# Kernel tuning notes

Measured on AMD Instinct MI355X. Metric: run time of the kernel, lower is better.

Reference implementation:

```python
import jax, jax.numpy as jnp
import numpy as np

OUT, IN, BLK, RANK = 4096, 4096, 32, 16
N_BLOCKS = IN // BLK  # 128
Q_ZERO = 128.0  # center of unsigned code range, maps codes to signed values


def setup_inputs() -> dict:
    key = jax.random.key(0)
    ks = jax.random.split(key, 6)
    x = jax.random.normal(ks[0], (4, 2048, IN), dtype=jnp.float32)
    # GGML-style block-quantized weight: int codes in blocks of 32 + per-block fp scale
    q_weight = jax.random.randint(ks[1], (OUT, N_BLOCKS, BLK), 0, 256, dtype=jnp.int32)
    scales = jax.random.uniform(ks[2], (OUT, N_BLOCKS), dtype=jnp.float32) * 0.02
    # LoRA patch applied to dequantized weight
    lora_up = jax.random.normal(ks[3], (OUT, RANK), dtype=jnp.float32) * 0.02
    lora_down = jax.random.normal(ks[4], (RANK, IN), dtype=jnp.float32) * 0.02
    bias = jax.random.normal(ks[5], (OUT,), dtype=jnp.float32)
    return {"x": x, "q_weight": q_weight, "scales": scales,
            "lora_up": lora_up, "lora_down": lora_down, "bias": bias}


def reference(x, q_weight, scales, lora_up, lora_down, bias):
    # 1) dequantize: per-block scale * centered int codes -> full fp weight [OUT, IN]
    w = (q_weight.astype(jnp.float32) - Q_ZERO) * scales[:, :, None]
    w = w.reshape(OUT, IN)
    # 2) apply LoRA patch to the dequantized weight (patch function in get_weight)
    w = w + lora_up @ lora_down
    # 3) delegate to the linear forward operation: y = x @ W^T + b
    return jnp.einsum('bsd,od->bso', x, w) + bias
```

## Files before the change

kernel.cpp:

```cpp
#include <hip/hip_runtime.h>
#include <cstdint>
#include <cstddef>

#define M_TOT 8192
#define N_TOT 4096
#define K_TOT 4096
#define RANK  16
#define BM 128
#define BN 128
#define BK 32

typedef float f32x4 __attribute__((ext_vector_type(4)));
typedef __bf16 bf16x8 __attribute__((ext_vector_type(8)));
typedef unsigned short u16x4 __attribute__((ext_vector_type(4)));

__device__ __forceinline__ unsigned short f32_to_bf16(float f) {
    union { float f; uint32_t u; } v; v.f = f;
    uint32_t r = v.u + (0x7fffu + ((v.u >> 16) & 1u));
    return (unsigned short)(r >> 16);
}

__device__ __forceinline__ void gload_lds16(const void* g, void* l) {
    __builtin_amdgcn_global_load_lds(
        (const __attribute__((address_space(1))) void*)g,
        (__attribute__((address_space(3))) void*)l,
        16, 0, 0);
}

__global__ __launch_bounds__(256) void convert_x_kernel(const float* __restrict__ x,
                                                        unsigned short* __restrict__ xb,
                                                        int n4) {
    int i = blockIdx.x * 256 + threadIdx.x;
    if (i >= n4) return;
    float4 v = ((const float4*)x)[i];
    u16x4 o;
    o.x = f32_to_bf16(v.x);
    o.y = f32_to_bf16(v.y);
    o.z = f32_to_bf16(v.z);
    o.w = f32_to_bf16(v.w);
    *(u16x4*)&xb[(size_t)i * 4] = o;
}

__global__ __launch_bounds__(256) void build_w_kernel(const int* __restrict__ q,
                                                      const float* __restrict__ scales,
                                                      const float* __restrict__ up,
                                                      const float* __restrict__ down,
                                                      unsigned short* __restrict__ W) {
    const int o = blockIdx.x;
    const int t = threadIdx.x;
    __shared__ float u[RANK];
    if (t < RANK) u[t] = up[o * RANK + t];
    __syncthreads();

    const int* qrow = q + (size_t)o * K_TOT;
    const float* srow = scales + (size_t)o * (K_TOT / 32);
    float acc[16];
#pragma unroll
    for (int i = 0; i < 16; i++) {
        int kk = t + 256 * i;
        acc[i] = ((float)qrow[kk] - 128.0f) * srow[kk >> 5];
    }
#pragma unroll
    for (int r = 0; r < RANK; r++) {
        float ur = u[r];
        const float* drow = down + (size_t)r * K_TOT;
#pragma unroll
        for (int i = 0; i < 16; i++) acc[i] += ur * drow[t + 256 * i];
    }
    unsigned short* wrow = W + (size_t)o * K_TOT;
#pragma unroll
    for (int i = 0; i < 16; i++) wrow[t + 256 * i] = f32_to_bf16(acc[i]);
}

__global__ __launch_bounds__(256) void gemm_bt_kernel(const unsigned short* __restrict__ A,
                                                      const unsigned short* __restrict__ B,
                                                      const float* __restrict__ bias,
                                                      float* __restrict__ C) {
    __shared__ unsigned short As[BM * BK];
    __shared__ unsigned short Bs[BN * BK];

    const int tid  = threadIdx.x;
    const int wave = tid >> 6;
    const int lane = tid & 63;
    const int wm = wave >> 1;
    const int wn = wave & 1;

    const int tile_m = (int)blockIdx.y * BM;
    const int tile_n = (int)blockIdx.x * BN;

    const int lrow = lane >> 2;
    const int lcol = (lane & 3) * 8;

    const int quad = lane >> 4;
    const int l16  = lane & 15;

    f32x4 acc[4][4];
#pragma unroll
    for (int i = 0; i < 4; i++)
#pragma unroll
        for (int j = 0; j < 4; j++) {
            f32x4 z = {0.f, 0.f, 0.f, 0.f};
            acc[i][j] = z;
        }

    for (int k0 = 0; k0 < K_TOT; k0 += BK) {
#pragma unroll
        for (int j = 0; j < 2; j++) {
            const int r0 = (j * 4 + wave) * 16;
            gload_lds16(A + (size_t)(tile_m + r0 + lrow) * K_TOT + (k0 + lcol), &As[r0 * BK]);
            gload_lds16(B + (size_t)(tile_n + r0 + lrow) * K_TOT + (k0 + lcol), &Bs[r0 * BK]);
        }
        __syncthreads();

        bf16x8 af[4], bfr[4];
#pragma unroll
        for (int mi = 0; mi < 4; mi++)
            af[mi] = *(const bf16x8*)&As[(wm * 64 + mi * 16 + l16) * BK + quad * 8];
#pragma unroll
        for (int ni = 0; ni < 4; ni++)
            bfr[ni] = *(const bf16x8*)&Bs[(wn * 64 + ni * 16 + l16) * BK + quad * 8];

#pragma unroll
        for (int mi = 0; mi < 4; mi++)
#pragma unroll
            for (int ni = 0; ni < 4; ni++)
                acc[mi][ni] = __builtin_amdgcn_mfma_f32_16x16x32_bf16(af[mi], bfr[ni], acc[mi][ni], 0, 0, 0);
        __syncthreads();
    }

#pragma unroll
    for (int ni = 0; ni < 4; ni++) {
        const int col = tile_n + wn * 64 + ni * 16 + l16;
        const float bv = bias[col];
#pragma unroll
        for (int mi = 0; mi < 4; mi++) {
#pragma unroll
            for (int r = 0; r < 4; r++) {
                const int row = tile_m + wm * 64 + mi * 16 + quad * 4 + r;
                C[(size_t)row * N_TOT + col] = acc[mi][ni][r] + bv;
            }
        }
    }
}

extern "C" void kernel_launch(void* const* d_in, const int* in_sizes, int n_in,
                              void* d_out, int out_size, void* d_ws, size_t ws_size,
                              hipStream_t stream) {
    const float* x      = (const float*)d_in[0];
    const int*   q      = (const int*)d_in[1];
    const float* scales = (const float*)d_in[2];
    const float* up     = (const float*)d_in[3];
    const float* down   = (const float*)d_in[4];
    const float* bias   = (const float*)d_in[5];
    float* out = (float*)d_out;

    unsigned short* xb = (unsigned short*)d_ws;
    unsigned short* wb = xb + (size_t)M_TOT * K_TOT;

    const int n4 = M_TOT * K_TOT / 4;
    convert_x_kernel<<<n4 / 256, 256, 0, stream>>>(x, xb, n4);
    build_w_kernel<<<N_TOT, 256, 0, stream>>>(q, scales, up, down, wb);
    gemm_bt_kernel<<<dim3(N_TOT / BN, M_TOT / BM), 256, 0, stream>>>(xb, wb, bias, out);
}
```

Baseline: 622.1 us.

## Swizzle GEMM LDS tiles, vectorize x conversion, batch four rows in weight build

```diff
diff --git a/kernel.cpp b/kernel.cpp
--- a/kernel.cpp
+++ b/kernel.cpp
@@ -12,7 +12,7 @@
 
 typedef float f32x4 __attribute__((ext_vector_type(4)));
 typedef __bf16 bf16x8 __attribute__((ext_vector_type(8)));
-typedef unsigned short u16x4 __attribute__((ext_vector_type(4)));
+typedef unsigned short u16x8 __attribute__((ext_vector_type(8)));
 
 __device__ __forceinline__ unsigned short f32_to_bf16(float f) {
     union { float f; uint32_t u; } v; v.f = f;
@@ -29,16 +29,17 @@
 
 __global__ __launch_bounds__(256) void convert_x_kernel(const float* __restrict__ x,
                                                         unsigned short* __restrict__ xb,
-                                                        int n4) {
+                                                        int n8) {
     int i = blockIdx.x * 256 + threadIdx.x;
-    if (i >= n4) return;
-    float4 v = ((const float4*)x)[i];
-    u16x4 o;
-    o.x = f32_to_bf16(v.x);
-    o.y = f32_to_bf16(v.y);
-    o.z = f32_to_bf16(v.z);
-    o.w = f32_to_bf16(v.w);
-    *(u16x4*)&xb[(size_t)i * 4] = o;
+    if (i >= n8) return;
+    float4 a = ((const float4*)x)[2 * (size_t)i];
+    float4 b = ((const float4*)x)[2 * (size_t)i + 1];
+    u16x8 o;
+    o[0] = f32_to_bf16(a.x); o[1] = f32_to_bf16(a.y);
+    o[2] = f32_to_bf16(a.z); o[3] = f32_to_bf16(a.w);
+    o[4] = f32_to_bf16(b.x); o[5] = f32_to_bf16(b.y);
+    o[6] = f32_to_bf16(b.z); o[7] = f32_to_bf16(b.w);
+    *(u16x8*)&xb[(size_t)i * 8] = o;
 }
 
 __global__ __launch_bounds__(256) void build_w_kernel(const int* __restrict__ q,
@@ -46,30 +47,53 @@
                                                       const float* __restrict__ up,
                                                       const float* __restrict__ down,
                                                       unsigned short* __restrict__ W) {
-    const int o = blockIdx.x;
+    const int o0 = blockIdx.x * 4;
     const int t = threadIdx.x;
-    __shared__ float u[RANK];
-    if (t < RANK) u[t] = up[o * RANK + t];
+    __shared__ float u[4][RANK];
+    if (t < 64) u[t >> 4][t & 15] = up[(o0 + (t >> 4)) * RANK + (t & 15)];
     __syncthreads();
 
-    const int* qrow = q + (size_t)o * K_TOT;
-    const float* srow = scales + (size_t)o * (K_TOT / 32);
-    float acc[16];
 #pragma unroll
-    for (int i = 0; i < 16; i++) {
-        int kk = t + 256 * i;
-        acc[i] = ((float)qrow[kk] - 128.0f) * srow[kk >> 5];
+    for (int cc = 0; cc < 2; cc++) {
+        const int c = t + 256 * cc;
+        const int k0 = c * 8;
+        float acc[4][8];
+#pragma unroll
+        for (int row = 0; row < 4; row++) {
+            const int o = o0 + row;
+            int4 qa = *(const int4*)&q[(size_t)o * K_TOT + k0];
+            int4 qb = *(const int4*)&q[(size_t)o * K_TOT + k0 + 4];
+            const float s = scales[o * (K_TOT / 32) + (k0 >> 5)];
+            acc[row][0] = (float)(qa.x - 128) * s;
+            acc[row][1] = (float)(qa.y - 128) * s;
+            acc[row][2] = (float)(qa.z - 128) * s;
+            acc[row][3] = (float)(qa.w - 128) * s;
+            acc[row][4] = (float)(qb.x - 128) * s;
+            acc[row][5] = (float)(qb.y - 128) * s;
+            acc[row][6] = (float)(qb.z - 128) * s;
+            acc[row][7] = (float)(qb.w - 128) * s;
+        }
+#pragma unroll
+        for (int r = 0; r < RANK; r++) {
+            float4 da = *(const float4*)&down[r * K_TOT + k0];
+            float4 db = *(const float4*)&down[r * K_TOT + k0 + 4];
+#pragma unroll
+            for (int row = 0; row < 4; row++) {
+                const float ur = u[row][r];
+                acc[row][0] += ur * da.x; acc[row][1] += ur * da.y;
+                acc[row][2] += ur * da.z; acc[row][3] += ur * da.w;
+                acc[row][4] += ur * db.x; acc[row][5] += ur * db.y;
+                acc[row][6] += ur * db.z; acc[row][7] += ur * db.w;
+            }
+        }
+#pragma unroll
+        for (int row = 0; row < 4; row++) {
+            u16x8 o8;
+#pragma unroll
+            for (int j = 0; j < 8; j++) o8[j] = f32_to_bf16(acc[row][j]);
+            *(u16x8*)&W[(size_t)(o0 + row) * K_TOT + k0] = o8;
+        }
     }
-#pragma unroll
-    for (int r = 0; r < RANK; r++) {
-        float ur = u[r];
-        const float* drow = down + (size_t)r * K_TOT;
-#pragma unroll
-        for (int i = 0; i < 16; i++) acc[i] += ur * drow[t + 256 * i];
-    }
-    unsigned short* wrow = W + (size_t)o * K_TOT;
-#pragma unroll
-    for (int i = 0; i < 16; i++) wrow[t + 256 * i] = f32_to_bf16(acc[i]);
 }
 
 __global__ __launch_bounds__(256) void gemm_bt_kernel(const unsigned short* __restrict__ A,
@@ -89,10 +113,11 @@
     const int tile_n = (int)blockIdx.x * BN;
 
     const int lrow = lane >> 2;
-    const int lcol = (lane & 3) * 8;
+    const int lcol = ((lane & 3) ^ ((lrow >> 1) & 3)) * 8;
 
     const int quad = lane >> 4;
     const int l16  = lane & 15;
+    const int swz  = (l16 >> 1) & 3;
 
     f32x4 acc[4][4];
 #pragma unroll
@@ -112,13 +137,14 @@
         }
         __syncthreads();
 
+        const int slot = (quad ^ swz) * 8;
         bf16x8 af[4], bfr[4];
 #pragma unroll
         for (int mi = 0; mi < 4; mi++)
-            af[mi] = *(const bf16x8*)&As[(wm * 64 + mi * 16 + l16) * BK + quad * 8];
+            af[mi] = *(const bf16x8*)&As[(wm * 64 + mi * 16 + l16) * BK + slot];
 #pragma unroll
         for (int ni = 0; ni < 4; ni++)
-            bfr[ni] = *(const bf16x8*)&Bs[(wn * 64 + ni * 16 + l16) * BK + quad * 8];
+            bfr[ni] = *(const bf16x8*)&Bs[(wn * 64 + ni * 16 + l16) * BK + slot];
 
 #pragma unroll
         for (int mi = 0; mi < 4; mi++)
@@ -157,8 +183,8 @@
     unsigned short* xb = (unsigned short*)d_ws;
     unsigned short* wb = xb + (size_t)M_TOT * K_TOT;
 
-    const int n4 = M_TOT * K_TOT / 4;
-    convert_x_kernel<<<n4 / 256, 256, 0, stream>>>(x, xb, n4);
-    build_w_kernel<<<N_TOT, 256, 0, stream>>>(q, scales, up, down, wb);
+    const int n8 = M_TOT * K_TOT / 8;
+    convert_x_kernel<<<n8 / 256, 256, 0, stream>>>(x, xb, n8);
+    build_w_kernel<<<N_TOT / 4, 256, 0, stream>>>(q, scales, up, down, wb);
     gemm_bt_kernel<<<dim3(N_TOT / BN, M_TOT / BM), 256, 0, stream>>>(xb, wb, bias, out);
 }
```

Measured after the change: 587.7 us. 5.5% less time.
